# Performance work log

Measured on AMD Instinct MI355X. Metric: run time of the kernel, lower is better.

## Reference

```python
import jax, jax.numpy as jnp
import numpy as np

B, T, IN, H = 64, 512, 512, 512


def _lstm_scan(x_tbd, h0, c0, Wih, Whh, b):
    """Run an LSTMCell over time. x_tbd: [T,B,IN]. Returns hs [T,B,H], (h,c)."""
    def step(carry, x):
        h, c = carry
        g = x @ Wih.T + h @ Whh.T + b          # [B, 4H], gates in torch order i,f,g,o
        i, f, gg, o = jnp.split(g, 4, axis=-1)
        i = jax.nn.sigmoid(i)
        f = jax.nn.sigmoid(f)
        gg = jnp.tanh(gg)
        o = jax.nn.sigmoid(o)
        c = f * c + i * gg
        h = o * jnp.tanh(c)
        return (h, c), h
    (h, c), hs = jax.lax.scan(step, (h0, c0), x_tbd)
    return hs, h, c


def setup_inputs() -> dict:
    key = jax.random.key(0)
    ks = jax.random.split(key, 9)
    s = 1.0 / np.sqrt(H)
    inp = {
        "input": jax.random.normal(ks[0], (B, T, IN), dtype=jnp.float32),
        "enc_h": jax.random.normal(ks[1], (B, 2 * H), dtype=jnp.float32),
        "enc_c": jax.random.normal(ks[2], (B, 2 * H), dtype=jnp.float32),
        "Wih_f": jax.random.uniform(ks[3], (4 * H, IN), jnp.float32, -s, s),
        "Whh_f": jax.random.uniform(ks[4], (4 * H, H), jnp.float32, -s, s),
        "b_f": jax.random.uniform(ks[5], (4 * H,), jnp.float32, -s, s),
        "Wih_b": jax.random.uniform(ks[6], (4 * H, IN), jnp.float32, -s, s),
        "Whh_b": jax.random.uniform(ks[7], (4 * H, H), jnp.float32, -s, s),
        "b_b": jax.random.uniform(ks[8], (4 * H,), jnp.float32, -s, s),
    }
    return inp


def reference(input, enc_h, enc_c, Wih_f, Whh_f, b_f, Wih_b, Whh_b, b_b):
    # split encoder state into forward / backward halves (num_layers=1)
    h0_f, h0_b = enc_h[:, :H], enc_h[:, H:]
    c0_f, c0_b = enc_c[:, :H], enc_c[:, H:]

    x_f = jnp.swapaxes(input, 0, 1)                 # [T,B,IN]
    x_b = jnp.swapaxes(jnp.flip(input, axis=1), 0, 1)

    out_f, h_f, c_f = _lstm_scan(x_f, h0_f, c0_f, Wih_f, Whh_f, b_f)
    out_b, h_b, c_b = _lstm_scan(x_b, h0_b, c0_b, Wih_b, Whh_b, b_b)

    out_f = jnp.swapaxes(out_f, 0, 1)               # [B,T,H]
    out_b = jnp.flip(jnp.swapaxes(out_b, 0, 1), axis=1)
    out = jnp.concatenate([out_f, out_b], axis=2)   # [B,T,2H]

    h = jnp.concatenate([h_f, h_b], axis=1)         # [B,2H]
    c = jnp.concatenate([c_f, c_b], axis=1)
    return out, h, c
```

## Files before the change

### kernel.cpp

```cpp
#include <hip/hip_runtime.h>

typedef _Float16 h8 __attribute__((ext_vector_type(8)));
typedef _Float16 h4 __attribute__((ext_vector_type(4)));
typedef float    f4 __attribute__((ext_vector_type(4)));
typedef unsigned u4 __attribute__((ext_vector_type(4)));

#define NT     512
#define OUT0   33554432

__device__ __forceinline__ float sigm(float x)  { return 1.0f / (1.0f + __expf(-x)); }
__device__ __forceinline__ float tanhf_(float x){ float e = __expf(2.0f * x); return 1.0f - 2.0f / (e + 1.0f); }


__global__ __launch_bounds__(256) void xconv_k(const float* __restrict__ x, _Float16* __restrict__ x16) {
    size_t i = ((size_t)blockIdx.x * 256 + threadIdx.x) * 4;
    f4 v = *(const f4*)(x + i);
    h4 o; o[0] = (_Float16)v[0]; o[1] = (_Float16)v[1]; o[2] = (_Float16)v[2]; o[3] = (_Float16)v[3];
    *(h4*)(x16 + i) = o;
}

__global__ __launch_bounds__(256) void wconv_k(const float* __restrict__ Wih_f, const float* __restrict__ Whh_f,
                                               const float* __restrict__ Wih_b, const float* __restrict__ Whh_b,
                                               _Float16* __restrict__ wcat) {
    size_t e = (size_t)blockIdx.x * 256 + threadIdx.x;
    int k4  = (int)(e & 255);
    int p   = (int)((e >> 8) & 2047);
    int dir = (int)(e >> 19);
    int gate = p & 3, j = p >> 2;
    int k = k4 * 4;
    const float* Wih = dir ? Wih_b : Wih_f;
    const float* Whh = dir ? Whh_b : Whh_f;
    f4 v;
    if (k < 512) v = *(const f4*)&Wih[((size_t)gate * 512 + j) * 512 + k];
    else         v = *(const f4*)&Whh[((size_t)gate * 512 + j) * 512 + (k - 512)];
    h4 o; o[0] = (_Float16)v[0]; o[1] = (_Float16)v[1]; o[2] = (_Float16)v[2]; o[3] = (_Float16)v[3];
    *(h4*)&wcat[(((size_t)dir * 2048) + p) * 1024 + k] = o;
}

__global__ __launch_bounds__(256) void initring_k(const float* __restrict__ enc_h, unsigned* __restrict__ rb) {
    int e = blockIdx.x * 256 + threadIdx.x;
    float v = enc_h[e];
    int b = e >> 10, q = e & 1023, dir = q >> 9, j = q & 511;
    unsigned short hb = __builtin_bit_cast(unsigned short, (_Float16)v);
    size_t idx = ((size_t)dir * 64 + b) * 512 + j;
    rb[idx]         = (unsigned)hb;
    rb[idx + 65536] = 0xFFFF0000u;
}

__global__ __launch_bounds__(256, 1) void lstm_persist(
    const _Float16* __restrict__ x16, const _Float16* __restrict__ wcat,
    const float* __restrict__ b_f, const float* __restrict__ b_b,
    const float* __restrict__ enc_c, unsigned* __restrict__ rb,
    float* __restrict__ out, float* __restrict__ hseg, float* __restrict__ cseg)
{
    const int bx  = blockIdx.x;
    const int grp = bx & 7;
    const int dir = grp >> 2, mg = grp & 3, ng = bx >> 3;
    const int b0 = mg * 16, p0 = ng * 64, j0 = ng * 16;
    const int tid = threadIdx.x, lane = tid & 63, kw = tid >> 6;
    const int l15 = lane & 15, koff = (lane >> 4) * 8;

    __shared__ float gbuf[2][4][16][68];

    f4 wx[4][4], wh[4][4];
    #pragma unroll
    for (int nt = 0; nt < 4; ++nt) {
        const _Float16* wrow = wcat + ((size_t)dir * 2048 + p0 + nt * 16 + l15) * 1024 + kw * 128 + koff;
        #pragma unroll
        for (int s = 0; s < 4; ++s) {
            wx[nt][s] = *(const f4*)(wrow + s * 32);
            wh[nt][s] = *(const f4*)(wrow + 512 + s * 32);
        }
    }
    #pragma unroll
    for (int nt = 0; nt < 4; ++nt)
        #pragma unroll
        for (int s = 0; s < 4; ++s) {
            asm volatile("" : "+v"(wx[nt][s]));
            asm volatile("" : "+v"(wh[nt][s]));
        }

    const int mb = tid >> 4, jj = tid & 15;
    const float* bias = dir ? b_b : b_f;
    const float bi = bias[0 * 512 + j0 + jj];
    const float bf = bias[1 * 512 + j0 + jj];
    const float bg = bias[2 * 512 + j0 + jj];
    const float bo = bias[3 * 512 + j0 + jj];
    float c = enc_c[(size_t)(b0 + mb) * 1024 + dir * 512 + j0 + jj];
    float hlast = 0.f;

    const _Float16* xbase = x16 + (size_t)(b0 + l15) * NT * 512 + kw * 128 + koff;

    f4 xf[4];
    {
        const _Float16* xp = xbase + (size_t)(dir ? (NT - 1) : 0) * 512;
        #pragma unroll
        for (int s = 0; s < 4; ++s) xf[s] = *(const f4*)(xp + s * 32);
    }

    const unsigned* pbase = rb + (size_t)dir * 32768 + (size_t)(b0 + l15) * 512 + kw * 128 + koff;
    unsigned* sbase = rb + (size_t)dir * 32768 + (size_t)(b0 + mb) * 512 + (j0 + jj);

    for (int t = 0; t < NT; ++t) {
        const int tx = dir ? (NT - 1 - t) : t;
        const unsigned* pp = pbase + (size_t)(t & 1) * 65536;

        u4 q0, q1, q2, q3, q4, q5, q6, q7;
        asm volatile(
            "global_load_dwordx4 %0, %8, off sc0 sc1\n\t"
            "global_load_dwordx4 %1, %8, off offset:16 sc0 sc1\n\t"
            "global_load_dwordx4 %2, %8, off offset:128 sc0 sc1\n\t"
            "global_load_dwordx4 %3, %8, off offset:144 sc0 sc1\n\t"
            "global_load_dwordx4 %4, %8, off offset:256 sc0 sc1\n\t"
            "global_load_dwordx4 %5, %8, off offset:272 sc0 sc1\n\t"
            "global_load_dwordx4 %6, %8, off offset:384 sc0 sc1\n\t"
            "global_load_dwordx4 %7, %8, off offset:400 sc0 sc1"
            : "=&v"(q0), "=&v"(q1), "=&v"(q2), "=&v"(q3),
              "=&v"(q4), "=&v"(q5), "=&v"(q6), "=&v"(q7)
            : "v"(pp) : "memory");

        f4 acc[4];
        #pragma unroll
        for (int nt = 0; nt < 4; ++nt) { acc[nt][0] = 0.f; acc[nt][1] = 0.f; acc[nt][2] = 0.f; acc[nt][3] = 0.f; }
        #pragma unroll
        for (int s = 0; s < 4; ++s) {
            h8 a = __builtin_bit_cast(h8, xf[s]);
            #pragma unroll
            for (int nt = 0; nt < 4; ++nt)
                acc[nt] = __builtin_amdgcn_mfma_f32_16x16x32_f16(a, __builtin_bit_cast(h8, wx[nt][s]), acc[nt], 0, 0, 0);
        }
        #pragma unroll
        for (int nt = 0; nt < 4; ++nt) asm volatile("" : "+v"(acc[nt]));
        __builtin_amdgcn_sched_barrier(0);

        const unsigned tagx = (unsigned)t << 16;
        for (;;) {
            asm volatile("s_waitcnt vmcnt(0)" ::: "memory");
            __builtin_amdgcn_sched_barrier(0);
            int ok = ((q0[0]^tagx)<0x10000u) & ((q0[1]^tagx)<0x10000u) & ((q0[2]^tagx)<0x10000u) & ((q0[3]^tagx)<0x10000u)
                   & ((q1[0]^tagx)<0x10000u) & ((q1[1]^tagx)<0x10000u) & ((q1[2]^tagx)<0x10000u) & ((q1[3]^tagx)<0x10000u)
                   & ((q2[0]^tagx)<0x10000u) & ((q2[1]^tagx)<0x10000u) & ((q2[2]^tagx)<0x10000u) & ((q2[3]^tagx)<0x10000u)
                   & ((q3[0]^tagx)<0x10000u) & ((q3[1]^tagx)<0x10000u) & ((q3[2]^tagx)<0x10000u) & ((q3[3]^tagx)<0x10000u)
                   & ((q4[0]^tagx)<0x10000u) & ((q4[1]^tagx)<0x10000u) & ((q4[2]^tagx)<0x10000u) & ((q4[3]^tagx)<0x10000u)
                   & ((q5[0]^tagx)<0x10000u) & ((q5[1]^tagx)<0x10000u) & ((q5[2]^tagx)<0x10000u) & ((q5[3]^tagx)<0x10000u)
                   & ((q6[0]^tagx)<0x10000u) & ((q6[1]^tagx)<0x10000u) & ((q6[2]^tagx)<0x10000u) & ((q6[3]^tagx)<0x10000u)
                   & ((q7[0]^tagx)<0x10000u) & ((q7[1]^tagx)<0x10000u) & ((q7[2]^tagx)<0x10000u) & ((q7[3]^tagx)<0x10000u);
            if (__all(ok)) break;
            asm volatile(
                "global_load_dwordx4 %0, %8, off sc0 sc1\n\t"
                "global_load_dwordx4 %1, %8, off offset:16 sc0 sc1\n\t"
                "global_load_dwordx4 %2, %8, off offset:128 sc0 sc1\n\t"
                "global_load_dwordx4 %3, %8, off offset:144 sc0 sc1\n\t"
                "global_load_dwordx4 %4, %8, off offset:256 sc0 sc1\n\t"
                "global_load_dwordx4 %5, %8, off offset:272 sc0 sc1\n\t"
                "global_load_dwordx4 %6, %8, off offset:384 sc0 sc1\n\t"
                "global_load_dwordx4 %7, %8, off offset:400 sc0 sc1\n\t"
                "s_waitcnt vmcnt(0)"
                : "=&v"(q0), "=&v"(q1), "=&v"(q2), "=&v"(q3),
                  "=&v"(q4), "=&v"(q5), "=&v"(q6), "=&v"(q7)
                : "v"(pp) : "memory");
        }

        if (t + 1 < NT) {
            const _Float16* xp = xbase + (size_t)(dir ? (NT - 2 - t) : (t + 1)) * 512;
            #pragma unroll
            for (int s = 0; s < 4; ++s) xf[s] = *(const f4*)(xp + s * 32);
        }

        h8 hfr[4];
        {
            u4 w;
            w[0] = (q0[0]&0xffffu)|(q0[1]<<16); w[1] = (q0[2]&0xffffu)|(q0[3]<<16);
            w[2] = (q1[0]&0xffffu)|(q1[1]<<16); w[3] = (q1[2]&0xffffu)|(q1[3]<<16);
            hfr[0] = __builtin_bit_cast(h8, w);
            w[0] = (q2[0]&0xffffu)|(q2[1]<<16); w[1] = (q2[2]&0xffffu)|(q2[3]<<16);
            w[2] = (q3[0]&0xffffu)|(q3[1]<<16); w[3] = (q3[2]&0xffffu)|(q3[3]<<16);
            hfr[1] = __builtin_bit_cast(h8, w);
            w[0] = (q4[0]&0xffffu)|(q4[1]<<16); w[1] = (q4[2]&0xffffu)|(q4[3]<<16);
            w[2] = (q5[0]&0xffffu)|(q5[1]<<16); w[3] = (q5[2]&0xffffu)|(q5[3]<<16);
            hfr[2] = __builtin_bit_cast(h8, w);
            w[0] = (q6[0]&0xffffu)|(q6[1]<<16); w[1] = (q6[2]&0xffffu)|(q6[3]<<16);
            w[2] = (q7[0]&0xffffu)|(q7[1]<<16); w[3] = (q7[2]&0xffffu)|(q7[3]<<16);
            hfr[3] = __builtin_bit_cast(h8, w);
        }

        #pragma unroll
        for (int s = 0; s < 4; ++s)
            #pragma unroll
            for (int nt = 0; nt < 4; ++nt)
                acc[nt] = __builtin_amdgcn_mfma_f32_16x16x32_f16(hfr[s], __builtin_bit_cast(h8, wh[nt][s]), acc[nt], 0, 0, 0);

        float (*gb)[16][68] = gbuf[t & 1];
        #pragma unroll
        for (int nt = 0; nt < 4; ++nt)
            #pragma unroll
            for (int r = 0; r < 4; ++r)
                gb[kw][(lane >> 4) * 4 + r][nt * 16 + l15] = acc[nt][r];
        __syncthreads();

        float gi = bi, gf = bf, gg = bg, go = bo;
        #pragma unroll
        for (int w = 0; w < 4; ++w) {
            gi += gb[w][mb][jj * 4 + 0];
            gf += gb[w][mb][jj * 4 + 1];
            gg += gb[w][mb][jj * 4 + 2];
            go += gb[w][mb][jj * 4 + 3];
        }
        float i_ = sigm(gi), f_ = sigm(gf), o_ = sigm(go), g_ = tanhf_(gg);
        c = f_ * c + i_ * g_;
        float h = o_ * tanhf_(c);
        hlast = h;

        {
            unsigned short hb = __builtin_bit_cast(unsigned short, (_Float16)h);
            unsigned uv = ((unsigned)(t + 1) << 16) | (unsigned)hb;
            unsigned* rd = sbase + (size_t)((t + 1) & 1) * 65536;
            asm volatile("global_store_dword %0, %1, off sc0 sc1" :: "v"(rd), "v"(uv) : "memory");
        }
        out[((size_t)(b0 + mb) * NT + tx) * 1024 + (size_t)(dir * 512 + j0 + jj)] = h;
    }

    asm volatile("s_waitcnt vmcnt(0)" ::: "memory");

    hseg[(size_t)(b0 + mb) * 1024 + dir * 512 + j0 + jj] = hlast;
    cseg[(size_t)(b0 + mb) * 1024 + dir * 512 + j0 + jj] = c;
}


extern "C" void kernel_launch(void* const* d_in, const int* in_sizes, int n_in,
                              void* d_out, int out_size, void* d_ws, size_t ws_size,
                              hipStream_t stream) {
    const float* xin   = (const float*)d_in[0];
    const float* enc_h = (const float*)d_in[1];
    const float* enc_c = (const float*)d_in[2];
    const float* Wih_f = (const float*)d_in[3];
    const float* Whh_f = (const float*)d_in[4];
    const float* b_f   = (const float*)d_in[5];
    const float* Wih_b = (const float*)d_in[6];
    const float* Whh_b = (const float*)d_in[7];
    const float* b_b   = (const float*)d_in[8];

    float* out  = (float*)d_out;
    float* hseg = out + OUT0;
    float* cseg = hseg + 65536;

    const size_t X16_BYTES  = (size_t)64 * 512 * 512 * 2;
    const size_t WCAT_BYTES = (size_t)2 * 2048 * 1024 * 2;

    _Float16* x16  = (_Float16*)d_ws;
    _Float16* wcat = (_Float16*)((char*)d_ws + X16_BYTES);
    unsigned* rb   = (unsigned*)((char*)d_ws + X16_BYTES + WCAT_BYTES);

    xconv_k<<<dim3(16384), dim3(256), 0, stream>>>(xin, x16);
    wconv_k<<<dim3(4096), dim3(256), 0, stream>>>(Wih_f, Whh_f, Wih_b, Whh_b, wcat);
    initring_k<<<dim3(256), dim3(256), 0, stream>>>(enc_h, rb);
    lstm_persist<<<dim3(256), dim3(256), 0, stream>>>(x16, wcat, b_f, b_b, enc_c,
                                                      rb, out, hseg, cseg);
}
```

Baseline: 2.027 ms.

## Duplicate recurrent-state ring with local-scope polling and system-scope fallback

```diff
diff --git a/kernel.cpp b/kernel.cpp
--- a/kernel.cpp
+++ b/kernel.cpp
@@ -37,20 +37,36 @@
     *(h4*)&wcat[(((size_t)dir * 2048) + p) * 1024 + k] = o;
 }
 
-__global__ __launch_bounds__(256) void initring_k(const float* __restrict__ enc_h, unsigned* __restrict__ rb) {
+__global__ __launch_bounds__(256) void initring_k(const float* __restrict__ enc_h,
+                                                  unsigned* __restrict__ rbL, unsigned* __restrict__ rbD) {
     int e = blockIdx.x * 256 + threadIdx.x;
     float v = enc_h[e];
     int b = e >> 10, q = e & 1023, dir = q >> 9, j = q & 511;
     unsigned short hb = __builtin_bit_cast(unsigned short, (_Float16)v);
     size_t idx = ((size_t)dir * 64 + b) * 512 + j;
-    rb[idx]         = (unsigned)hb;
-    rb[idx + 65536] = 0xFFFF0000u;
-}
+    rbL[idx] = (unsigned)hb;  rbL[idx + 65536] = 0xFFFF0000u;
+    rbD[idx] = (unsigned)hb;  rbD[idx + 65536] = 0xFFFF0000u;
+}
+
+#define ISSUE_POLL(pp, SC)                                             \
+    asm volatile(                                                      \
+        "global_load_dwordx4 %0, %8, off " SC "\n\t"                   \
+        "global_load_dwordx4 %1, %8, off offset:16 " SC "\n\t"         \
+        "global_load_dwordx4 %2, %8, off offset:128 " SC "\n\t"        \
+        "global_load_dwordx4 %3, %8, off offset:144 " SC "\n\t"        \
+        "global_load_dwordx4 %4, %8, off offset:256 " SC "\n\t"        \
+        "global_load_dwordx4 %5, %8, off offset:272 " SC "\n\t"        \
+        "global_load_dwordx4 %6, %8, off offset:384 " SC "\n\t"        \
+        "global_load_dwordx4 %7, %8, off offset:400 " SC               \
+        : "=&v"(q0), "=&v"(q1), "=&v"(q2), "=&v"(q3),                  \
+          "=&v"(q4), "=&v"(q5), "=&v"(q6), "=&v"(q7)                   \
+        : "v"(pp) : "memory")
 
 __global__ __launch_bounds__(256, 1) void lstm_persist(
     const _Float16* __restrict__ x16, const _Float16* __restrict__ wcat,
     const float* __restrict__ b_f, const float* __restrict__ b_b,
-    const float* __restrict__ enc_c, unsigned* __restrict__ rb,
+    const float* __restrict__ enc_c,
+    unsigned* __restrict__ rbL, unsigned* __restrict__ rbD,
     float* __restrict__ out, float* __restrict__ hseg, float* __restrict__ cseg)
 {
     const int bx  = blockIdx.x;
@@ -98,26 +114,18 @@
         for (int s = 0; s < 4; ++s) xf[s] = *(const f4*)(xp + s * 32);
     }
 
-    const unsigned* pbase = rb + (size_t)dir * 32768 + (size_t)(b0 + l15) * 512 + kw * 128 + koff;
-    unsigned* sbase = rb + (size_t)dir * 32768 + (size_t)(b0 + mb) * 512 + (j0 + jj);
+    const size_t roff  = (size_t)dir * 32768 + (size_t)(b0 + l15) * 512 + kw * 128 + koff;
+    const size_t soff  = (size_t)dir * 32768 + (size_t)(b0 + mb) * 512 + (j0 + jj);
+    const unsigned* pbL = rbL + roff;
+    const unsigned* pbD = rbD + roff;
+    unsigned* sbL = rbL + soff;
+    unsigned* sbD = rbD + soff;
+
+    int fb = 0;
 
     for (int t = 0; t < NT; ++t) {
         const int tx = dir ? (NT - 1 - t) : t;
-        const unsigned* pp = pbase + (size_t)(t & 1) * 65536;
-
-        u4 q0, q1, q2, q3, q4, q5, q6, q7;
-        asm volatile(
-            "global_load_dwordx4 %0, %8, off sc0 sc1\n\t"
-            "global_load_dwordx4 %1, %8, off offset:16 sc0 sc1\n\t"
-            "global_load_dwordx4 %2, %8, off offset:128 sc0 sc1\n\t"
-            "global_load_dwordx4 %3, %8, off offset:144 sc0 sc1\n\t"
-            "global_load_dwordx4 %4, %8, off offset:256 sc0 sc1\n\t"
-            "global_load_dwordx4 %5, %8, off offset:272 sc0 sc1\n\t"
-            "global_load_dwordx4 %6, %8, off offset:384 sc0 sc1\n\t"
-            "global_load_dwordx4 %7, %8, off offset:400 sc0 sc1"
-            : "=&v"(q0), "=&v"(q1), "=&v"(q2), "=&v"(q3),
-              "=&v"(q4), "=&v"(q5), "=&v"(q6), "=&v"(q7)
-            : "v"(pp) : "memory");
+        const size_t slot = (size_t)(t & 1) * 65536;
 
         f4 acc[4];
         #pragma unroll
@@ -133,7 +141,12 @@
         for (int nt = 0; nt < 4; ++nt) asm volatile("" : "+v"(acc[nt]));
         __builtin_amdgcn_sched_barrier(0);
 
+        const unsigned* ppL = pbL + slot;
+        const unsigned* ppD = pbD + slot;
         const unsigned tagx = (unsigned)t << 16;
+        u4 q0, q1, q2, q3, q4, q5, q6, q7;
+        if (!fb) { ISSUE_POLL(ppL, "sc0"); } else { ISSUE_POLL(ppD, "sc0 sc1"); }
+        int rounds = 0;
         for (;;) {
             asm volatile("s_waitcnt vmcnt(0)" ::: "memory");
             __builtin_amdgcn_sched_barrier(0);
@@ -146,19 +159,8 @@
                    & ((q6[0]^tagx)<0x10000u) & ((q6[1]^tagx)<0x10000u) & ((q6[2]^tagx)<0x10000u) & ((q6[3]^tagx)<0x10000u)
                    & ((q7[0]^tagx)<0x10000u) & ((q7[1]^tagx)<0x10000u) & ((q7[2]^tagx)<0x10000u) & ((q7[3]^tagx)<0x10000u);
             if (__all(ok)) break;
-            asm volatile(
-                "global_load_dwordx4 %0, %8, off sc0 sc1\n\t"
-                "global_load_dwordx4 %1, %8, off offset:16 sc0 sc1\n\t"
-                "global_load_dwordx4 %2, %8, off offset:128 sc0 sc1\n\t"
-                "global_load_dwordx4 %3, %8, off offset:144 sc0 sc1\n\t"
-                "global_load_dwordx4 %4, %8, off offset:256 sc0 sc1\n\t"
-                "global_load_dwordx4 %5, %8, off offset:272 sc0 sc1\n\t"
-                "global_load_dwordx4 %6, %8, off offset:384 sc0 sc1\n\t"
-                "global_load_dwordx4 %7, %8, off offset:400 sc0 sc1\n\t"
-                "s_waitcnt vmcnt(0)"
-                : "=&v"(q0), "=&v"(q1), "=&v"(q2), "=&v"(q3),
-                  "=&v"(q4), "=&v"(q5), "=&v"(q6), "=&v"(q7)
-                : "v"(pp) : "memory");
+            if (!fb && (++rounds >= 64)) fb = 1;
+            if (!fb) { ISSUE_POLL(ppL, "sc0"); } else { ISSUE_POLL(ppD, "sc0 sc1"); }
         }
 
         if (t + 1 < NT) {
@@ -214,8 +216,11 @@
         {
             unsigned short hb = __builtin_bit_cast(unsigned short, (_Float16)h);
             unsigned uv = ((unsigned)(t + 1) << 16) | (unsigned)hb;
-            unsigned* rd = sbase + (size_t)((t + 1) & 1) * 65536;
-            asm volatile("global_store_dword %0, %1, off sc0 sc1" :: "v"(rd), "v"(uv) : "memory");
+            const size_t nslot = (size_t)((t + 1) & 1) * 65536;
+            unsigned* rdD = sbD + nslot;
+            unsigned* rdL = sbL + nslot;
+            asm volatile("global_store_dword %0, %1, off sc0 sc1" :: "v"(rdD), "v"(uv) : "memory");
+            asm volatile("global_store_dword %0, %1, off sc0"     :: "v"(rdL), "v"(uv) : "memory");
         }
         out[((size_t)(b0 + mb) * NT + tx) * 1024 + (size_t)(dir * 512 + j0 + jj)] = h;
     }
@@ -246,14 +251,16 @@
 
     const size_t X16_BYTES  = (size_t)64 * 512 * 512 * 2;
     const size_t WCAT_BYTES = (size_t)2 * 2048 * 1024 * 2;
+    const size_t RING_BYTES = (size_t)2 * 65536 * 4;
 
     _Float16* x16  = (_Float16*)d_ws;
     _Float16* wcat = (_Float16*)((char*)d_ws + X16_BYTES);
-    unsigned* rb   = (unsigned*)((char*)d_ws + X16_BYTES + WCAT_BYTES);
+    unsigned* rbL  = (unsigned*)((char*)d_ws + X16_BYTES + WCAT_BYTES);
+    unsigned* rbD  = (unsigned*)((char*)d_ws + X16_BYTES + WCAT_BYTES + RING_BYTES);
 
     xconv_k<<<dim3(16384), dim3(256), 0, stream>>>(xin, x16);
     wconv_k<<<dim3(4096), dim3(256), 0, stream>>>(Wih_f, Whh_f, Wih_b, Whh_b, wcat);
-    initring_k<<<dim3(256), dim3(256), 0, stream>>>(enc_h, rb);
+    initring_k<<<dim3(256), dim3(256), 0, stream>>>(enc_h, rbL, rbD);
     lstm_persist<<<dim3(256), dim3(256), 0, stream>>>(x16, wcat, b_f, b_b, enc_c,
-                                                      rb, out, hseg, cseg);
-}
+                                                      rbL, rbD, out, hseg, cseg);
+}
```

Measured after the change: 2.129 ms. 1.05x slower.

## Poll canary words before full h reload and remap block indices

Applied to the files above, without the earlier changes.

```diff
diff --git a/kernel.cpp b/kernel.cpp
--- a/kernel.cpp
+++ b/kernel.cpp
@@ -47,6 +47,55 @@
     rb[idx + 65536] = 0xFFFF0000u;
 }
 
+#define ISSUE_FULL_NOWAIT(pp)                                           \
+    asm volatile(                                                       \
+        "global_load_dwordx4 %0, %8, off sc0 sc1\n\t"                   \
+        "global_load_dwordx4 %1, %8, off offset:16 sc0 sc1\n\t"         \
+        "global_load_dwordx4 %2, %8, off offset:128 sc0 sc1\n\t"        \
+        "global_load_dwordx4 %3, %8, off offset:144 sc0 sc1\n\t"        \
+        "global_load_dwordx4 %4, %8, off offset:256 sc0 sc1\n\t"        \
+        "global_load_dwordx4 %5, %8, off offset:272 sc0 sc1\n\t"        \
+        "global_load_dwordx4 %6, %8, off offset:384 sc0 sc1\n\t"        \
+        "global_load_dwordx4 %7, %8, off offset:400 sc0 sc1"            \
+        : "=&v"(q0), "=&v"(q1), "=&v"(q2), "=&v"(q3),                   \
+          "=&v"(q4), "=&v"(q5), "=&v"(q6), "=&v"(q7)                    \
+        : "v"(pp) : "memory")
+
+#define ISSUE_FULL_WAIT(pp)                                             \
+    asm volatile(                                                       \
+        "global_load_dwordx4 %0, %8, off sc0 sc1\n\t"                   \
+        "global_load_dwordx4 %1, %8, off offset:16 sc0 sc1\n\t"         \
+        "global_load_dwordx4 %2, %8, off offset:128 sc0 sc1\n\t"        \
+        "global_load_dwordx4 %3, %8, off offset:144 sc0 sc1\n\t"        \
+        "global_load_dwordx4 %4, %8, off offset:256 sc0 sc1\n\t"        \
+        "global_load_dwordx4 %5, %8, off offset:272 sc0 sc1\n\t"        \
+        "global_load_dwordx4 %6, %8, off offset:384 sc0 sc1\n\t"        \
+        "global_load_dwordx4 %7, %8, off offset:400 sc0 sc1\n\t"        \
+        "s_waitcnt vmcnt(0)"                                            \
+        : "=&v"(q0), "=&v"(q1), "=&v"(q2), "=&v"(q3),                   \
+          "=&v"(q4), "=&v"(q5), "=&v"(q6), "=&v"(q7)                    \
+        : "v"(pp) : "memory")
+
+#define ISSUE_CANARY_WAIT(pp)                                           \
+    asm volatile(                                                       \
+        "global_load_dword %0, %4, off sc0 sc1\n\t"                     \
+        "global_load_dword %1, %4, off offset:128 sc0 sc1\n\t"          \
+        "global_load_dword %2, %4, off offset:256 sc0 sc1\n\t"          \
+        "global_load_dword %3, %4, off offset:384 sc0 sc1\n\t"          \
+        "s_waitcnt vmcnt(0)"                                            \
+        : "=&v"(c0), "=&v"(c1), "=&v"(c2), "=&v"(c3)                    \
+        : "v"(pp) : "memory")
+
+#define TAGS_OK()                                                                                                  \
+    ( ((q0[0]^tagx)<0x10000u) & ((q0[1]^tagx)<0x10000u) & ((q0[2]^tagx)<0x10000u) & ((q0[3]^tagx)<0x10000u)        \
+    & ((q1[0]^tagx)<0x10000u) & ((q1[1]^tagx)<0x10000u) & ((q1[2]^tagx)<0x10000u) & ((q1[3]^tagx)<0x10000u)        \
+    & ((q2[0]^tagx)<0x10000u) & ((q2[1]^tagx)<0x10000u) & ((q2[2]^tagx)<0x10000u) & ((q2[3]^tagx)<0x10000u)        \
+    & ((q3[0]^tagx)<0x10000u) & ((q3[1]^tagx)<0x10000u) & ((q3[2]^tagx)<0x10000u) & ((q3[3]^tagx)<0x10000u)        \
+    & ((q4[0]^tagx)<0x10000u) & ((q4[1]^tagx)<0x10000u) & ((q4[2]^tagx)<0x10000u) & ((q4[3]^tagx)<0x10000u)        \
+    & ((q5[0]^tagx)<0x10000u) & ((q5[1]^tagx)<0x10000u) & ((q5[2]^tagx)<0x10000u) & ((q5[3]^tagx)<0x10000u)        \
+    & ((q6[0]^tagx)<0x10000u) & ((q6[1]^tagx)<0x10000u) & ((q6[2]^tagx)<0x10000u) & ((q6[3]^tagx)<0x10000u)        \
+    & ((q7[0]^tagx)<0x10000u) & ((q7[1]^tagx)<0x10000u) & ((q7[2]^tagx)<0x10000u) & ((q7[3]^tagx)<0x10000u) )
+
 __global__ __launch_bounds__(256, 1) void lstm_persist(
     const _Float16* __restrict__ x16, const _Float16* __restrict__ wcat,
     const float* __restrict__ b_f, const float* __restrict__ b_b,
@@ -54,8 +103,7 @@
     float* __restrict__ out, float* __restrict__ hseg, float* __restrict__ cseg)
 {
     const int bx  = blockIdx.x;
-    const int grp = bx & 7;
-    const int dir = grp >> 2, mg = grp & 3, ng = bx >> 3;
+    const int dir = bx >> 7, mg = (bx >> 5) & 3, ng = bx & 31;
     const int b0 = mg * 16, p0 = ng * 64, j0 = ng * 16;
     const int tid = threadIdx.x, lane = tid & 63, kw = tid >> 6;
     const int l15 = lane & 15, koff = (lane >> 4) * 8;
@@ -101,23 +149,20 @@
     const unsigned* pbase = rb + (size_t)dir * 32768 + (size_t)(b0 + l15) * 512 + kw * 128 + koff;
     unsigned* sbase = rb + (size_t)dir * 32768 + (size_t)(b0 + mb) * 512 + (j0 + jj);
 
+    int spec = 1;
+
     for (int t = 0; t < NT; ++t) {
         const int tx = dir ? (NT - 1 - t) : t;
         const unsigned* pp = pbase + (size_t)(t & 1) * 65536;
+        const unsigned tagx = (unsigned)t << 16;
 
         u4 q0, q1, q2, q3, q4, q5, q6, q7;
-        asm volatile(
-            "global_load_dwordx4 %0, %8, off sc0 sc1\n\t"
-            "global_load_dwordx4 %1, %8, off offset:16 sc0 sc1\n\t"
-            "global_load_dwordx4 %2, %8, off offset:128 sc0 sc1\n\t"
-            "global_load_dwordx4 %3, %8, off offset:144 sc0 sc1\n\t"
-            "global_load_dwordx4 %4, %8, off offset:256 sc0 sc1\n\t"
-            "global_load_dwordx4 %5, %8, off offset:272 sc0 sc1\n\t"
-            "global_load_dwordx4 %6, %8, off offset:384 sc0 sc1\n\t"
-            "global_load_dwordx4 %7, %8, off offset:400 sc0 sc1"
-            : "=&v"(q0), "=&v"(q1), "=&v"(q2), "=&v"(q3),
-              "=&v"(q4), "=&v"(q5), "=&v"(q6), "=&v"(q7)
-            : "v"(pp) : "memory");
+        unsigned c0, c1, c2, c3;
+
+        if (spec) {
+            ISSUE_FULL_NOWAIT(pp);
+            __builtin_amdgcn_sched_barrier(0);
+        }
 
         f4 acc[4];
         #pragma unroll
@@ -133,33 +178,26 @@
         for (int nt = 0; nt < 4; ++nt) asm volatile("" : "+v"(acc[nt]));
         __builtin_amdgcn_sched_barrier(0);
 
-        const unsigned tagx = (unsigned)t << 16;
-        for (;;) {
+        int rounds = 0;
+        int allok = 0;
+        if (spec) {
             asm volatile("s_waitcnt vmcnt(0)" ::: "memory");
             __builtin_amdgcn_sched_barrier(0);
-            int ok = ((q0[0]^tagx)<0x10000u) & ((q0[1]^tagx)<0x10000u) & ((q0[2]^tagx)<0x10000u) & ((q0[3]^tagx)<0x10000u)
-                   & ((q1[0]^tagx)<0x10000u) & ((q1[1]^tagx)<0x10000u) & ((q1[2]^tagx)<0x10000u) & ((q1[3]^tagx)<0x10000u)
-                   & ((q2[0]^tagx)<0x10000u) & ((q2[1]^tagx)<0x10000u) & ((q2[2]^tagx)<0x10000u) & ((q2[3]^tagx)<0x10000u)
-                   & ((q3[0]^tagx)<0x10000u) & ((q3[1]^tagx)<0x10000u) & ((q3[2]^tagx)<0x10000u) & ((q3[3]^tagx)<0x10000u)
-                   & ((q4[0]^tagx)<0x10000u) & ((q4[1]^tagx)<0x10000u) & ((q4[2]^tagx)<0x10000u) & ((q4[3]^tagx)<0x10000u)
-                   & ((q5[0]^tagx)<0x10000u) & ((q5[1]^tagx)<0x10000u) & ((q5[2]^tagx)<0x10000u) & ((q5[3]^tagx)<0x10000u)
-                   & ((q6[0]^tagx)<0x10000u) & ((q6[1]^tagx)<0x10000u) & ((q6[2]^tagx)<0x10000u) & ((q6[3]^tagx)<0x10000u)
-                   & ((q7[0]^tagx)<0x10000u) & ((q7[1]^tagx)<0x10000u) & ((q7[2]^tagx)<0x10000u) & ((q7[3]^tagx)<0x10000u);
-            if (__all(ok)) break;
-            asm volatile(
-                "global_load_dwordx4 %0, %8, off sc0 sc1\n\t"
-                "global_load_dwordx4 %1, %8, off offset:16 sc0 sc1\n\t"
-                "global_load_dwordx4 %2, %8, off offset:128 sc0 sc1\n\t"
-                "global_load_dwordx4 %3, %8, off offset:144 sc0 sc1\n\t"
-                "global_load_dwordx4 %4, %8, off offset:256 sc0 sc1\n\t"
-                "global_load_dwordx4 %5, %8, off offset:272 sc0 sc1\n\t"
-                "global_load_dwordx4 %6, %8, off offset:384 sc0 sc1\n\t"
-                "global_load_dwordx4 %7, %8, off offset:400 sc0 sc1\n\t"
-                "s_waitcnt vmcnt(0)"
-                : "=&v"(q0), "=&v"(q1), "=&v"(q2), "=&v"(q3),
-                  "=&v"(q4), "=&v"(q5), "=&v"(q6), "=&v"(q7)
-                : "v"(pp) : "memory");
-        }
+            allok = __all(TAGS_OK());
+        }
+        while (!allok) {
+            for (;;) {
+                ISSUE_CANARY_WAIT(pp);
+                int cok = ((c0^tagx)<0x10000u) & ((c1^tagx)<0x10000u)
+                        & ((c2^tagx)<0x10000u) & ((c3^tagx)<0x10000u);
+                if (__all(cok)) break;
+                ++rounds;
+            }
+            ISSUE_FULL_WAIT(pp);
+            allok = __all(TAGS_OK());
+            ++rounds;
+        }
+        spec = (rounds <= 1);
 
         if (t + 1 < NT) {
             const _Float16* xp = xbase + (size_t)(dir ? (NT - 2 - t) : (t + 1)) * 512;
```

Result: slower. 2.530 ms (+24.8%).
